# Optimization experiments

Measured on AMD Instinct MI355X. Metric: run time of the kernel, lower is better.

The kernel has to match this reference:

```python
import jax, jax.numpy as jnp
import numpy as np
from jax import lax

OUT_SIZE = 224  # original input spatial size (output_size of anomaly map)
NUM_NEIGHBORS = 9
SIGMA = 4.0
KSIZE = 2 * int(4.0 * SIGMA + 0.5) + 1  # 33, kornia-style kernel size


def avg_pool3(x):
    # AvgPool2d(3, 1, 1), count_include_pad=True -> sum over 3x3 window / 9
    s = lax.reduce_window(x, 0.0, lax.add, (1, 1, 3, 3), (1, 1, 1, 1),
                          [(0, 0), (0, 0), (1, 1), (1, 1)])
    return s / 9.0


def euclidean_dist(x, y):
    # x: [..., N, E], y: [..., M, E] -> [..., N, M]
    x_norm = jnp.sum(x * x, axis=-1, keepdims=True)
    y_norm = jnp.sum(y * y, axis=-1, keepdims=True)
    res = x_norm - 2.0 * jnp.matmul(x, jnp.swapaxes(y, -2, -1)) + jnp.swapaxes(y_norm, -2, -1)
    return jnp.sqrt(jnp.clip(res, 0.0))


def gaussian_blur(x):
    # x: [B,1,H,W]; separable Gaussian, reflect padding (kornia GaussianBlur2d default)
    r = KSIZE // 2
    t = jnp.arange(KSIZE, dtype=x.dtype) - r
    k = jnp.exp(-(t * t) / (2.0 * SIGMA * SIGMA))
    k = k / jnp.sum(k)
    xp = jnp.pad(x, ((0, 0), (0, 0), (r, r), (r, r)), mode='reflect')
    kh = k.reshape(1, 1, KSIZE, 1)
    kw = k.reshape(1, 1, 1, KSIZE)
    y = lax.conv_general_dilated(xp, kh, (1, 1), 'VALID',
                                 dimension_numbers=('NCHW', 'OIHW', 'NCHW'))
    return lax.conv_general_dilated(y, kw, (1, 1), 'VALID',
                                    dimension_numbers=('NCHW', 'OIHW', 'NCHW'))


def compute_anomaly_score(patch_scores, locations, embedding, memory_bank):
    # patch_scores/locations: [B, P]; embedding: [B*P, E]; memory_bank: [M, E]
    batch, num_patches = patch_scores.shape
    bidx = jnp.arange(batch)
    max_patches = jnp.argmax(patch_scores, axis=1)                       # [B]
    max_feats = embedding.reshape(batch, num_patches, -1)[bidx, max_patches]  # [B,E]
    score = patch_scores[bidx, max_patches]                              # [B]
    nn_index = locations[bidx, max_patches]                              # [B]
    nn_sample = memory_bank[nn_index]                                    # [B,E]
    n_nb = min(NUM_NEIGHBORS, memory_bank.shape[0])
    d_bank = euclidean_dist(nn_sample, memory_bank)                      # [B,M]
    _, support = lax.top_k(-d_bank, n_nb)                                # [B,k] smallest
    sup_feats = memory_bank[support]                                     # [B,k,E]
    d = euclidean_dist(max_feats[:, None, :], sup_feats)[:, 0, :]        # [B,k]
    weights = (1.0 - jax.nn.softmax(d, axis=1))[:, 0]                    # [B]
    return weights * score


def setup_inputs() -> dict:
    key = jax.random.key(0)
    k1, k2, k3 = jax.random.split(key, 3)
    feat2 = jax.random.normal(k1, (8, 512, 28, 28), dtype=jnp.float32)
    feat3 = jax.random.normal(k2, (8, 1024, 14, 14), dtype=jnp.float32)
    memory_bank = jax.random.normal(k3, (20000, 1536), dtype=jnp.float32)
    return {'feat2': feat2, 'feat3': feat3, 'memory_bank': memory_bank}


def reference(feat2, feat3, memory_bank):
    # feature pooling (AvgPool2d(3,1,1) on each backbone layer)
    f2 = avg_pool3(feat2)
    f3 = avg_pool3(feat3)
    batch, _, height, width = f2.shape
    # generate_embedding: bilinear upsample deeper layer, concat along channels
    f3u = jax.image.resize(f3, (batch, f3.shape[1], height, width), method='bilinear')
    emb = jnp.concatenate([f2, f3u], axis=1)                 # [B,1536,28,28]
    emb_dim = emb.shape[1]
    embedding = emb.transpose(0, 2, 3, 1).reshape(-1, emb_dim)  # [B*784, 1536]
    # nearest_neighbors with n_neighbors=1
    dist = euclidean_dist(embedding, memory_bank)            # [N, M]
    patch_scores = jnp.min(dist, axis=1)
    locations = jnp.argmin(dist, axis=1)
    patch_scores = patch_scores.reshape(batch, -1)
    locations = locations.reshape(batch, -1)
    pred_score = compute_anomaly_score(patch_scores, locations, embedding, memory_bank)
    # anomaly map: bilinear upsample patch scores to input size + gaussian blur
    score_map = patch_scores.reshape(batch, 1, width, height)
    amap = jax.image.resize(score_map, (batch, 1, OUT_SIZE, OUT_SIZE), method='bilinear')
    anomaly_map = gaussian_blur(amap)
    return anomaly_map, pred_score
```

## Files before the change

kernel.cpp:

```cpp
#include <hip/hip_runtime.h>
#include <math.h>

#define NB 8
#define C2 512
#define C3 1024
#define H2 28
#define W2 28
#define H3 14
#define W3 14
#define EDIM 1536
#define PPB (H2*W2)
#define NPATCH (NB*PPB)
#define MPAD 6400
#define MBANK 20000
#define NBPAD 20096
#define NBG (NBPAD/16)
#define OUTW 224
#define NNB 9
#define KS 33
#define KR 16
#define NMT 25
#define NNTB 157
#define CHUNKS 8
#define CH (MBANK/CHUNKS)
#define MPB 64
#define NSLAB 24
#define GRPB (NSLAB*1024)

#define SXQ 63.5f
#define SYQ (127.0f/6.0f)

typedef __attribute__((ext_vector_type(4))) int   i32x4;

#define LEXLT(va,ia,vb,ib) ((va) < (vb) || ((va)==(vb) && (ia)<(ib)))
#define CSWAP(va,ia,vb,ib) { if (LEXLT(va,ia,vb,ib)) { float _tv=(vb); int _ti=(ib); (vb)=(va); (ib)=(ia); (va)=_tv; (ia)=_ti; } }

#define BAR() asm volatile("s_barrier" ::: "memory")
#define WAITV6() asm volatile("s_waitcnt vmcnt(6)" ::: "memory")
#define WAITV0() asm volatile("s_waitcnt vmcnt(0)" ::: "memory")

__device__ __forceinline__ void gload16(const void* g, void* l) {
  __builtin_amdgcn_global_load_lds(
      (const __attribute__((address_space(1))) unsigned int*)g,
      (__attribute__((address_space(3))) unsigned int*)l, 16, 0, 0);
}
__device__ __forceinline__ signed char q8(float x, float s) {
  int v = (int)rintf(x * s);
  v = v > 127 ? 127 : (v < -127 ? -127 : v);
  return (signed char)v;
}
__device__ __forceinline__ size_t pk_addr(int row, int c) {
  return ((size_t)((row >> 4)*NSLAB + (c >> 6)) << 10)
       + (((c >> 4) & 3) << 8) + ((row & 15) << 4) + (c & 15);
}


__global__ __launch_bounds__(256) void pool2_kernel(const float* __restrict__ in,
    float* __restrict__ emb32, signed char* __restrict__ embp) {
  int bid = blockIdx.x;
  int cg = bid & 7; int h = (bid >> 3) % H2; int b = bid / (8*H2);
  int t = threadIdx.x;
  __shared__ float s3[3][64][29];
  for (int li = t; li < 3*64*28; li += 256) {
    int w = li % 28; int c = (li/28) & 63; int dh = li/(28*64);
    int hh = h + dh - 1;
    float v = 0.f;
    if (hh >= 0 && hh < H2) v = in[((size_t)(b*C2) + cg*64 + c)*784 + hh*28 + w];
    s3[dh][c][w] = v;
  }
  __syncthreads();
  for (int o = t; o < 64*28; o += 256) {
    int c = o & 63, w = o >> 6;
    float s = 0.f;
    #pragma unroll
    for (int dh = 0; dh < 3; ++dh) {
      s += s3[dh][c][w];
      if (w > 0)  s += s3[dh][c][w-1];
      if (w < 27) s += s3[dh][c][w+1];
    }
    s *= (1.f/9.f);
    int row = b*PPB + h*28 + w;
    int cc = cg*64 + c;
    emb32[(size_t)row*EDIM + cc] = s;
    embp[pk_addr(row, cc)] = q8(s, SXQ);
  }
}

__global__ void pool3_kernel(const float* __restrict__ in, float* __restrict__ f3p) {
  int id = blockIdx.x*blockDim.x + threadIdx.x;
  if (id >= NB*C3*H3*W3) return;
  int w = id % W3, h = (id / W3) % H3, c = (id / (H3*W3)) % C3, b = id / (C3*H3*W3);
  const float* src = in + (size_t)(b*C3 + c)*H3*W3;
  float s = 0.f;
  #pragma unroll
  for (int dh=-1; dh<=1; ++dh) {
    int hh = h+dh; if (hh<0||hh>=H3) continue;
    #pragma unroll
    for (int dw=-1; dw<=1; ++dw) {
      int ww = w+dw; if (ww<0||ww>=W3) continue;
      s += src[hh*W3+ww];
    }
  }
  f3p[(size_t)id] = s * (1.f/9.f);
}

__global__ __launch_bounds__(256) void up3_kernel(const float* __restrict__ f3p,
    float* __restrict__ emb32, signed char* __restrict__ embp) {
  int bid = blockIdx.x;
  int cg = bid & 15; int i = (bid >> 4) % H2; int b = bid / (16*H2);
  int t = threadIdx.x;
  float sy = i*0.5f - 0.25f; sy = fminf(fmaxf(sy,0.f),(float)(H3-1));
  int y0 = (int)sy; int y1 = min(y0+1,H3-1); float fy = sy - (float)y0;
  __shared__ float r2[2][64][15];
  for (int li = t; li < 2*64*14; li += 256) {
    int w = li % 14; int c = (li/14) & 63; int yy = li/(14*64);
    int ysrc = yy ? y1 : y0;
    r2[yy][c][w] = f3p[((size_t)(b*C3) + cg*64 + c)*196 + ysrc*14 + w];
  }
  __syncthreads();
  for (int o = t; o < 64*28; o += 256) {
    int c = o & 63, j = o >> 6;
    float sx = j*0.5f - 0.25f; sx = fminf(fmaxf(sx,0.f),(float)(W3-1));
    int x0 = (int)sx; int x1 = min(x0+1,W3-1); float fx = sx - (float)x0;
    float v = (1.f-fy)*((1.f-fx)*r2[0][c][x0] + fx*r2[0][c][x1])
            +      fy *((1.f-fx)*r2[1][c][x0] + fx*r2[1][c][x1]);
    int row = b*PPB + i*28 + j;
    int cc = C2 + cg*64 + c;
    emb32[(size_t)row*EDIM + cc] = v;
    embp[pk_addr(row, cc)] = q8(v, SXQ);
  }
}


__global__ __launch_bounds__(256) void bank_pack_kernel(const float* __restrict__ bank,
                                                        signed char* __restrict__ bankp,
                                                        float* __restrict__ yn) {
  __shared__ float rn[16];
  int grp = blockIdx.x;
  int t = threadIdx.x;
  if (t < 16) rn[t] = 0.f;
  __syncthreads();
  #pragma unroll
  for (int q = 0; q < 6; ++q) {
    int chunk = t + 256*q;
    int p = chunk >> 6, l = chunk & 63;
    int h = l & 15, gg = l >> 4;
    int row = grp*16 + h;
    int o16[4] = {0,0,0,0};
    if (row < MBANK) {
      const float* src = bank + (size_t)row*EDIM + p*64 + gg*16;
      signed char* oc = (signed char*)o16;
      float ls = 0.f;
      #pragma unroll
      for (int e = 0; e < 16; ++e) { float v = src[e]; ls = fmaf(v, v, ls); oc[e] = q8(v, SYQ); }
      atomicAdd(&rn[h], ls);
    }
    *reinterpret_cast<int4*>(bankp + (size_t)grp*GRPB + (size_t)chunk*16) =
        make_int4(o16[0], o16[1], o16[2], o16[3]);
  }
  __syncthreads();
  if (t < 16 && grp*16 + t < MBANK) yn[grp*16 + t] = rn[t];
}


__global__ __launch_bounds__(512, 4) void dist_min_i8(
    const signed char* __restrict__ Apk, const signed char* __restrict__ Bpk,
    const float* __restrict__ yn, float* __restrict__ outq, int* __restrict__ outi)
{
  __shared__ __align__(16) unsigned char LDSC[49152];
  const int t = threadIdx.x;
  const int lane = t & 63, wid = t >> 6;
  const int wr = wid >> 1, wc = wid & 1;

  const int nwg = NMT*NNTB;
  int orig = blockIdx.x;
  int xcd = orig & 7, loc = orig >> 3;
  int qq = nwg >> 3, rm = nwg & 7;
  int wg = (xcd < rm ? xcd*(qq+1) : rm*(qq+1) + (xcd-rm)*qq) + loc;
  const int mt = wg / NNTB, nt = wg % NNTB;
  const int m0 = mt*256, n0 = nt*128;

  const int gA = (m0 >> 4) + wid*2;
  const signed char* aSrc0 = Apk + (size_t)gA*GRPB + lane*16;
  const signed char* aSrc1 = Apk + (size_t)(gA+1)*GRPB + lane*16;
  const unsigned aDstOff = (unsigned)(wid*2048);

  const signed char* bp[4];
  #pragma unroll
  for (int j = 0; j < 4; ++j) {
    int n16 = (n0 >> 4) + wc*4 + j;
    bp[j] = Bpk + (size_t)n16*GRPB + lane*16;
  }
  const unsigned aRd = (unsigned)((wr*4)*1024 + lane*16);

  i32x4 acc[4][4];
  #pragma unroll
  for (int i = 0; i < 4; ++i)
    #pragma unroll
    for (int j = 0; j < 4; ++j) acc[i][j] = (i32x4){0,0,0,0};

  i32x4 bfv0[4], bfv1[4];

  gload16(aSrc0, (char*)LDSC + aDstOff);
  gload16(aSrc1, (char*)LDSC + aDstOff + 1024);
  gload16(aSrc0 + 1024, (char*)LDSC + 16384u + aDstOff);
  gload16(aSrc1 + 1024, (char*)LDSC + 16384u + aDstOff + 1024);
  #pragma unroll
  for (int j = 0; j < 4; ++j) bfv0[j] = *(const i32x4*)(bp[j]);
  WAITV6();
  BAR();

  #pragma unroll 2
  for (int p = 0; p < NSLAB; ++p) {
    const unsigned sb = (unsigned)(p % 3) * 16384u;
    const bool even = (p & 1) == 0;
    if (p < NSLAB-1) {
      if (even) {
        #pragma unroll
        for (int j = 0; j < 4; ++j) bfv1[j] = *(const i32x4*)(bp[j] + (size_t)(p+1)*1024);
      } else {
        #pragma unroll
        for (int j = 0; j < 4; ++j) bfv0[j] = *(const i32x4*)(bp[j] + (size_t)(p+1)*1024);
      }
    }
    if (p < NSLAB-2) {
      const unsigned sw = (unsigned)((p+2) % 3) * 16384u;
      gload16(aSrc0 + (size_t)(p+2)*1024, (char*)LDSC + sw + aDstOff);
      gload16(aSrc1 + (size_t)(p+2)*1024, (char*)LDSC + sw + aDstOff + 1024);
    }
    i32x4 af[4];
    #pragma unroll
    for (int i = 0; i < 4; ++i)
      af[i] = *(const i32x4*)(LDSC + sb + aRd + i*1024);
    __builtin_amdgcn_s_setprio(1);
    if (even) {
      #pragma unroll
      for (int i = 0; i < 4; ++i)
        #pragma unroll
        for (int j = 0; j < 4; ++j)
          acc[i][j] = __builtin_amdgcn_mfma_i32_16x16x64_i8(af[i], bfv0[j], acc[i][j], 0, 0, 0);
    } else {
      #pragma unroll
      for (int i = 0; i < 4; ++i)
        #pragma unroll
        for (int j = 0; j < 4; ++j)
          acc[i][j] = __builtin_amdgcn_mfma_i32_16x16x64_i8(af[i], bfv1[j], acc[i][j], 0, 0, 0);
    }
    __builtin_amdgcn_s_setprio(0);
    if (p < NSLAB-2) { WAITV6(); } else { WAITV0(); }
    BAR();
  }

  const float NEG2INV = -2.0f * (2.0f/127.0f) * (6.0f/127.0f);
  const int h = lane & 15, g = lane >> 4;
  float ynv[4];
  #pragma unroll
  for (int j = 0; j < 4; ++j) {
    int col = n0 + wc*64 + j*16 + h;
    ynv[j] = col < MBANK ? yn[col] : INFINITY;
  }
  float* smin = (float*)LDSC;
  int* sidx = (int*)(LDSC + 2048);
  #pragma unroll
  for (int i = 0; i < 4; ++i) {
    #pragma unroll
    for (int r = 0; r < 4; ++r) {
      float v = INFINITY; int ix = 0x7fffffff;
      #pragma unroll
      for (int j = 0; j < 4; ++j) {
        float q = fmaf(NEG2INV, (float)acc[i][j][r], ynv[j]);
        int col = n0 + wc*64 + j*16 + h;
        if (q < v || (q == v && col < ix)) { v = q; ix = col; }
      }
      #pragma unroll
      for (int m = 1; m < 16; m <<= 1) {
        float ov = __shfl_xor(v, m);
        int   oi = __shfl_xor(ix, m);
        if (ov < v || (ov == v && oi < ix)) { v = ov; ix = oi; }
      }
      if (h == 0) {
        int rl = wr*64 + i*16 + g*4 + r;
        smin[rl*2 + wc] = v;
        sidx[rl*2 + wc] = ix;
      }
    }
  }
  __syncthreads();
  if (t < 256) {
    float v0 = smin[t*2], v1 = smin[t*2+1];
    int   i0 = sidx[t*2], i1 = sidx[t*2+1];
    float v; int ix;
    if (LEXLT(v1, i1, v0, i0)) { v = v1; ix = i1; } else { v = v0; ix = i0; }
    int row = m0 + t;
    if (row < NPATCH) {
      outq[(size_t)nt*NPATCH + row] = v;
      outi[(size_t)nt*NPATCH + row] = ix;
    }
  }
}


__global__ __launch_bounds__(256) void minrescore_kernel(
    const float* __restrict__ outq, const int* __restrict__ outi,
    const float* __restrict__ emb32, const float* __restrict__ bank,
    const float* __restrict__ yn, int* __restrict__ loc, float* __restrict__ ps) {
  int w = (blockIdx.x*blockDim.x + threadIdx.x) >> 6;
  int lane = threadIdx.x & 63;
  if (w >= NPATCH) return;
  float bv = INFINITY; int bi = 0x7fffffff;
  for (int s = lane; s < NNTB; s += 64) {
    float v = outq[(size_t)s*NPATCH + w];
    int  ix = outi[(size_t)s*NPATCH + w];
    if (LEXLT(v, ix, bv, bi)) { bv = v; bi = ix; }
  }
  #pragma unroll
  for (int m = 32; m; m >>= 1) {
    float ov = __shfl_xor(bv, m);
    int   oi = __shfl_xor(bi, m);
    if (LEXLT(ov, oi, bv, bi)) { bv = ov; bi = oi; }
  }
  int j = bi;
  if (lane == 0) loc[w] = j;
  const float4* x = reinterpret_cast<const float4*>(emb32 + (size_t)w*EDIM);
  const float4* y = reinterpret_cast<const float4*>(bank + (size_t)j*EDIM);
  float accd = 0.f, accx = 0.f;
  #pragma unroll
  for (int k = 0; k < EDIM/4/64; ++k) {
    float4 a = x[lane + k*64], b = y[lane + k*64];
    accd = fmaf(a.x,b.x,accd); accd = fmaf(a.y,b.y,accd);
    accd = fmaf(a.z,b.z,accd); accd = fmaf(a.w,b.w,accd);
    accx = fmaf(a.x,a.x,accx); accx = fmaf(a.y,a.y,accx);
    accx = fmaf(a.z,a.z,accx); accx = fmaf(a.w,a.w,accx);
  }
  #pragma unroll
  for (int s = 32; s; s >>= 1) { accd += __shfl_xor(accd, s); accx += __shfl_xor(accx, s); }
  if (lane == 0) ps[w] = sqrtf(fmaxf(accx - 2.f*accd + yn[j], 0.f));
}


__global__ void argmax_kernel(const float* __restrict__ ps, const int* __restrict__ loc,
                              float* __restrict__ bscore, int* __restrict__ brow, int* __restrict__ bnn) {
  __shared__ float sv[256]; __shared__ int si[256];
  int b = blockIdx.x, t = threadIdx.x;
  float bv = -INFINITY; int bi = 0x7fffffff;
  for (int p = t; p < PPB; p += 256) {
    float v = ps[b*PPB + p];
    if (v > bv || (v == bv && p < bi)) { bv = v; bi = p; }
  }
  sv[t] = bv; si[t] = bi; __syncthreads();
  for (int s = 128; s; s >>= 1) {
    if (t < s) {
      if (sv[t+s] > sv[t] || (sv[t+s] == sv[t] && si[t+s] < si[t])) { sv[t] = sv[t+s]; si[t] = si[t+s]; }
    }
    __syncthreads();
  }
  if (t == 0) {
    bscore[b] = sv[0];
    brow[b]   = b*PPB + si[0];
    bnn[b]    = loc[b*PPB + si[0]];
  }
}

__global__ __launch_bounds__(256) void dbank_kernel(
    const float* __restrict__ bank, const float* __restrict__ yn,
    const int* __restrict__ bnn, float* __restrict__ dbank)
{
  __shared__ float xs[8][EDIM];
  int t = threadIdx.x;
  for (int idx = t*4; idx < 8*EDIM; idx += 256*4) {
    int b = idx / EDIM, k = idx % EDIM;
    float4 v = *reinterpret_cast<const float4*>(bank + (size_t)bnn[b]*EDIM + k);
    *reinterpret_cast<float4*>(&xs[b][k]) = v;
  }
  __syncthreads();
  int lane = t & 63, w = t >> 6;
  for (int u = 0; u < MPB/4; ++u) {
    int m = blockIdx.x*MPB + u*4 + w;
    if (m < MBANK) {
      const float4* yp = reinterpret_cast<const float4*>(bank + (size_t)m*EDIM);
      float acc[8] = {0.f,0.f,0.f,0.f,0.f,0.f,0.f,0.f};
      for (int k4 = lane; k4 < EDIM/4; k4 += 64) {
        float4 y = yp[k4];
        int k = k4*4;
        #pragma unroll
        for (int b = 0; b < 8; ++b) {
          acc[b] = fmaf(y.x, xs[b][k+0], acc[b]);
          acc[b] = fmaf(y.y, xs[b][k+1], acc[b]);
          acc[b] = fmaf(y.z, xs[b][k+2], acc[b]);
          acc[b] = fmaf(y.w, xs[b][k+3], acc[b]);
        }
      }
      #pragma unroll
      for (int b = 0; b < 8; ++b) {
        float a = acc[b];
        #pragma unroll
        for (int s = 32; s; s >>= 1) a += __shfl_xor(a, s);
        acc[b] = a;
      }
      if (lane == 0) {
        #pragma unroll
        for (int b = 0; b < 8; ++b) {
          int nn = bnn[b];
          float d2 = yn[nn] - 2.f*acc[b] + yn[m];
          dbank[(size_t)b*MBANK + m] = sqrtf(fmaxf(d2, 0.f));
        }
      }
    }
  }
}


__global__ __launch_bounds__(256) void top9_stage1(const float* __restrict__ dbank,
                                                   float* __restrict__ cv, int* __restrict__ ci) {
  int b = blockIdx.x / CHUNKS, ch = blockIdx.x % CHUNKS;
  const float* db = dbank + (size_t)b*MBANK + ch*CH;
  int t = threadIdx.x;

  float v0=INFINITY,v1=INFINITY,v2=INFINITY,v3=INFINITY,v4=INFINITY,
        v5=INFINITY,v6=INFINITY,v7=INFINITY,v8=INFINITY;
  int i0=0x7fffffff,i1=0x7fffffff,i2=0x7fffffff,i3=0x7fffffff,i4=0x7fffffff,
      i5=0x7fffffff,i6=0x7fffffff,i7=0x7fffffff,i8=0x7fffffff;

  for (int s = 0; s < (CH+255)/256; ++s) {
    int m = t + s*256;
    if (m < CH) {
      float nv = db[m]; int ni = ch*CH + m;
      if (LEXLT(nv,ni,v8,i8)) {
        v8 = nv; i8 = ni;
        CSWAP(v8,i8,v7,i7); CSWAP(v7,i7,v6,i6); CSWAP(v6,i6,v5,i5); CSWAP(v5,i5,v4,i4);
        CSWAP(v4,i4,v3,i3); CSWAP(v3,i3,v2,i2); CSWAP(v2,i2,v1,i1); CSWAP(v1,i1,v0,i0);
      }
    }
  }

  __shared__ float sv[256*9];
  __shared__ int   si[256*9];
  __shared__ float rv[256]; __shared__ int ri[256]; __shared__ int rp[256];
  sv[t*9+0]=v0; sv[t*9+1]=v1; sv[t*9+2]=v2; sv[t*9+3]=v3; sv[t*9+4]=v4;
  sv[t*9+5]=v5; sv[t*9+6]=v6; sv[t*9+7]=v7; sv[t*9+8]=v8;
  si[t*9+0]=i0; si[t*9+1]=i1; si[t*9+2]=i2; si[t*9+3]=i3; si[t*9+4]=i4;
  si[t*9+5]=i5; si[t*9+6]=i6; si[t*9+7]=i7; si[t*9+8]=i8;
  __syncthreads();

  for (int r = 0; r < NNB; ++r) {
    float bv = INFINITY; int bix = 0x7fffffff; int bp = -1;
    #pragma unroll
    for (int u = 0; u < 9; ++u) {
      float v = sv[t*9+u]; int ix = si[t*9+u];
      if (LEXLT(v,ix,bv,bix)) { bv = v; bix = ix; bp = t*9+u; }
    }
    rv[t] = bv; ri[t] = bix; rp[t] = bp; __syncthreads();
    for (int s = 128; s; s >>= 1) {
      if (t < s) {
        if (LEXLT(rv[t+s],ri[t+s],rv[t],ri[t])) { rv[t]=rv[t+s]; ri[t]=ri[t+s]; rp[t]=rp[t+s]; }
      }
      __syncthreads();
    }
    if (t == 0) {
      cv[blockIdx.x*NNB + r] = rv[0];
      ci[blockIdx.x*NNB + r] = ri[0];
      sv[rp[0]] = INFINITY; si[rp[0]] = 0x7fffffff;
    }
    __syncthreads();
  }
}


__global__ __launch_bounds__(128) void finalize_kernel(
    const float* __restrict__ cv, const int* __restrict__ ci,
    const float* __restrict__ emb32, const float* __restrict__ bank,
    const float* __restrict__ yn, const int* __restrict__ brow,
    const float* __restrict__ bscore, float* __restrict__ out) {
  __shared__ float sv[128]; __shared__ int si[128];
  __shared__ float wv[128]; __shared__ int wi[128]; __shared__ int wp[128];
  __shared__ int supp[NNB]; __shared__ float ds[NNB];
  int b = blockIdx.x, t = threadIdx.x;
  if (t < CHUNKS*NNB) { sv[t] = cv[b*CHUNKS*NNB + t]; si[t] = ci[b*CHUNKS*NNB + t]; }
  else { sv[t] = INFINITY; si[t] = 0x7fffffff; }
  __syncthreads();
  for (int r = 0; r < NNB; ++r) {
    wv[t] = sv[t]; wi[t] = si[t]; wp[t] = t; __syncthreads();
    for (int s = 64; s; s >>= 1) {
      if (t < s) {
        if (LEXLT(wv[t+s],wi[t+s],wv[t],wi[t])) { wv[t]=wv[t+s]; wi[t]=wi[t+s]; wp[t]=wp[t+s]; }
      }
      __syncthreads();
    }
    if (t == 0) {
      supp[r] = wi[0];
      sv[wp[0]] = INFINITY; si[wp[0]] = 0x7fffffff;
    }
    __syncthreads();
  }
  int lane = t & 63, w = t >> 6;
  int row = brow[b];
  const float* x = emb32 + (size_t)row*EDIM;
  for (int j = w; j < NNB; j += 2) {
    const float* y = bank + (size_t)supp[j]*EDIM;
    float accd = 0.f, accx = 0.f;
    for (int k = lane; k < EDIM; k += 64) {
      float a = x[k];
      accd = fmaf(a, y[k], accd);
      accx = fmaf(a, a, accx);
    }
    #pragma unroll
    for (int s = 32; s; s >>= 1) { accd += __shfl_xor(accd, s); accx += __shfl_xor(accx, s); }
    if (lane == 0) ds[j] = sqrtf(fmaxf(accx - 2.f*accd + yn[supp[j]], 0.f));
  }
  __syncthreads();
  if (t == 0) {
    float mx = -INFINITY;
    #pragma unroll
    for (int j = 0; j < NNB; ++j) mx = fmaxf(mx, ds[j]);
    float s = 0.f;
    #pragma unroll
    for (int j = 0; j < NNB; ++j) s += expf(ds[j] - mx);
    float wgt = 1.f - expf(ds[0] - mx) / s;
    out[b] = wgt * bscore[b];
  }
}


__device__ __forceinline__ int refl224(int x) {
  if (x < 0) return -x;
  if (x > OUTW-1) return 2*(OUTW-1) - x;
  return x;
}

__global__ __launch_bounds__(256) void upblurh_kernel(const float* __restrict__ ps,
                                                      float* __restrict__ tmp) {
  int b = blockIdx.x / OUTW, i = blockIdx.x % OUTW;
  int t = threadIdx.x;
  __shared__ float l[W2];
  __shared__ float graw[KS];
  if (t < KS) {
    float x = (float)t - (float)KR;
    graw[t] = expf(-(x*x) / (2.f*4.f*4.f));
  }
  float sy = ((float)i + 0.5f)*0.125f - 0.5f; sy = fminf(fmaxf(sy,0.f),(float)(H2-1));
  int y0 = (int)sy; int y1 = min(y0+1,H2-1); float fy = sy - (float)y0;
  if (t < W2) {
    const float* p = ps + b*PPB;
    l[t] = (1.f-fy)*p[y0*W2+t] + fy*p[y1*W2+t];
  }
  __syncthreads();
  if (t >= OUTW) return;
  float gsum = 0.f;
  #pragma unroll
  for (int u = 0; u < KS; ++u) gsum += graw[u];
  float winv = 1.f / gsum;
  float s = 0.f;
  #pragma unroll
  for (int v = 0; v < KS; ++v) {
    int jj = refl224(t - KR + v);
    float sx = ((float)jj + 0.5f)*0.125f - 0.5f; sx = fminf(fmaxf(sx,0.f),(float)(W2-1));
    int x0 = (int)sx; int x1 = min(x0+1,W2-1); float fx = sx - (float)x0;
    s = fmaf(graw[v]*winv, (1.f-fx)*l[x0] + fx*l[x1], s);
  }
  tmp[((size_t)b*OUTW + i)*OUTW + t] = s;
}

__global__ __launch_bounds__(256) void blurv_kernel(const float* __restrict__ in,
                                                    float* __restrict__ out) {
  __shared__ float graw[KS];
  int t = threadIdx.x;
  if (t < KS) {
    float x = (float)t - (float)KR;
    graw[t] = expf(-(x*x) / (2.f*4.f*4.f));
  }
  __syncthreads();
  int id = blockIdx.x*blockDim.x + t;
  if (id >= NB*OUTW*OUTW) return;
  float gsum = 0.f;
  #pragma unroll
  for (int u = 0; u < KS; ++u) gsum += graw[u];
  float winv = 1.f / gsum;
  int j = id % OUTW, i = (id/OUTW) % OUTW, b = id/(OUTW*OUTW);
  float s = 0.f;
  #pragma unroll
  for (int u = 0; u < KS; ++u) {
    int ii = refl224(i - KR + u);
    s = fmaf(graw[u]*winv, in[((size_t)b*OUTW + ii)*OUTW + j], s);
  }
  out[id] = s;
}


extern "C" void kernel_launch(void* const* d_in, const int* in_sizes, int n_in,
                              void* d_out, int out_size, void* d_ws, size_t ws_size,
                              hipStream_t stream) {
  const float* feat2 = (const float*)d_in[0];
  const float* feat3 = (const float*)d_in[1];
  const float* bank  = (const float*)d_in[2];
  float* out = (float*)d_out;

  char* base = (char*)d_ws;
  size_t off = 0;
  auto alloc = [&](size_t nbytes) -> char* {
    char* p = base + off;
    off += ((nbytes + 255) & ~(size_t)255);
    return p;
  };
  float*       emb32 = (float*)      alloc((size_t)NPATCH*EDIM*4);
  signed char* embp  = (signed char*)alloc((size_t)(MPAD/16)*GRPB);
  signed char* bankp = (signed char*)alloc((size_t)NBG*GRPB);
  float* f3p    = (float*)alloc((size_t)NB*C3*H3*W3*4);
  float* yn     = (float*)alloc(MBANK*4);
  float* outq   = (float*)alloc((size_t)NNTB*NPATCH*4);
  int*   outi   = (int*)  alloc((size_t)NNTB*NPATCH*4);
  float* ps     = (float*)alloc(NPATCH*4);
  int*   loc    = (int*)  alloc(NPATCH*4);
  float* bscore = (float*)alloc(NB*4);
  int*   brow   = (int*)  alloc(NB*4);
  int*   bnn    = (int*)  alloc(NB*4);
  float* dbank  = (float*)alloc((size_t)NB*MBANK*4);
  float* cv     = (float*)alloc(NB*CHUNKS*NNB*4);
  int*   ci     = (int*)  alloc(NB*CHUNKS*NNB*4);
  float* tmp    = (float*)alloc((size_t)NB*OUTW*OUTW*4);

  pool2_kernel<<<NB*H2*8, 256, 0, stream>>>(feat2, emb32, embp);
  {
    int n = NB*C3*H3*W3;
    pool3_kernel<<<(n+255)/256, 256, 0, stream>>>(feat3, f3p);
  }
  up3_kernel<<<NB*H2*16, 256, 0, stream>>>(f3p, emb32, embp);
  bank_pack_kernel<<<NBG, 256, 0, stream>>>(bank, bankp, yn);

  dist_min_i8<<<NMT*NNTB, 512, 0, stream>>>(embp, bankp, yn, outq, outi);
  minrescore_kernel<<<(NPATCH*64)/256, 256, 0, stream>>>(outq, outi, emb32, bank, yn, loc, ps);

  argmax_kernel<<<NB, 256, 0, stream>>>(ps, loc, bscore, brow, bnn);
  dbank_kernel<<<(MBANK+MPB-1)/MPB, 256, 0, stream>>>(bank, yn, bnn, dbank);
  top9_stage1<<<NB*CHUNKS, 256, 0, stream>>>(dbank, cv, ci);
  finalize_kernel<<<NB, 128, 0, stream>>>(cv, ci, emb32, bank, yn, brow, bscore,
                                          out + NB*OUTW*OUTW);

  {
    upblurh_kernel<<<NB*OUTW, 256, 0, stream>>>(ps, tmp);
    int n = NB*OUTW*OUTW;
    blurv_kernel<<<(n+255)/256, 256, 0, stream>>>(tmp, out);
  }
}
```

Before: 485.5 us.

## Fuse argmax into rescore via atomic keys and fuse dbank with per-block top-9

Replaces the separate per-batch argmax kernel with a packed 64-bit atomicMax issued from the rescore kernel. The bank-distance computation is fused with a per-block top-9 selection, so the 8x20000 distance matrix is never written to global memory. The two-stage top-9 merge is collapsed into the finalize kernel. This removes two launches and one global round trip, but adds atomics, a memset, and a larger candidate list (313 blocks x 9) for finalize to merge serially.

```diff
diff --git a/kernel.cpp b/kernel.cpp
--- a/kernel.cpp
+++ b/kernel.cpp
@@ -21,8 +21,7 @@
 #define KR 16
 #define NMT 25
 #define NNTB 157
-#define CHUNKS 8
-#define CH (MBANK/CHUNKS)
+#define NBLK 313
 #define MPB 64
 #define NSLAB 24
 #define GRPB (NSLAB*1024)
@@ -174,9 +173,9 @@
 
   const int nwg = NMT*NNTB;
   int orig = blockIdx.x;
-  int xcd = orig & 7, loc = orig >> 3;
+  int xcd = orig & 7, loc_ = orig >> 3;
   int qq = nwg >> 3, rm = nwg & 7;
-  int wg = (xcd < rm ? xcd*(qq+1) : rm*(qq+1) + (xcd-rm)*qq) + loc;
+  int wg = (xcd < rm ? xcd*(qq+1) : rm*(qq+1) + (xcd-rm)*qq) + loc_;
   const int mt = wg / NNTB, nt = wg % NNTB;
   const int m0 = mt*256, n0 = nt*128;
 
@@ -303,7 +302,8 @@
 __global__ __launch_bounds__(256) void minrescore_kernel(
     const float* __restrict__ outq, const int* __restrict__ outi,
     const float* __restrict__ emb32, const float* __restrict__ bank,
-    const float* __restrict__ yn, int* __restrict__ loc, float* __restrict__ ps) {
+    const float* __restrict__ yn, int* __restrict__ loc, float* __restrict__ ps,
+    unsigned long long* __restrict__ keys) {
   int w = (blockIdx.x*blockDim.x + threadIdx.x) >> 6;
   int lane = threadIdx.x & 63;
   if (w >= NPATCH) return;
@@ -320,7 +320,6 @@
     if (LEXLT(ov, oi, bv, bi)) { bv = ov; bi = oi; }
   }
   int j = bi;
-  if (lane == 0) loc[w] = j;
   const float4* x = reinterpret_cast<const float4*>(emb32 + (size_t)w*EDIM);
   const float4* y = reinterpret_cast<const float4*>(bank + (size_t)j*EDIM);
   float accd = 0.f, accx = 0.f;
@@ -334,48 +333,43 @@
   }
   #pragma unroll
   for (int s = 32; s; s >>= 1) { accd += __shfl_xor(accd, s); accx += __shfl_xor(accx, s); }
-  if (lane == 0) ps[w] = sqrtf(fmaxf(accx - 2.f*accd + yn[j], 0.f));
-}
-
-
-__global__ void argmax_kernel(const float* __restrict__ ps, const int* __restrict__ loc,
-                              float* __restrict__ bscore, int* __restrict__ brow, int* __restrict__ bnn) {
-  __shared__ float sv[256]; __shared__ int si[256];
-  int b = blockIdx.x, t = threadIdx.x;
-  float bv = -INFINITY; int bi = 0x7fffffff;
-  for (int p = t; p < PPB; p += 256) {
-    float v = ps[b*PPB + p];
-    if (v > bv || (v == bv && p < bi)) { bv = v; bi = p; }
-  }
-  sv[t] = bv; si[t] = bi; __syncthreads();
-  for (int s = 128; s; s >>= 1) {
-    if (t < s) {
-      if (sv[t+s] > sv[t] || (sv[t+s] == sv[t] && si[t+s] < si[t])) { sv[t] = sv[t+s]; si[t] = si[t+s]; }
-    }
-    __syncthreads();
-  }
-  if (t == 0) {
-    bscore[b] = sv[0];
-    brow[b]   = b*PPB + si[0];
-    bnn[b]    = loc[b*PPB + si[0]];
-  }
-}
-
-__global__ __launch_bounds__(256) void dbank_kernel(
+  if (lane == 0) {
+    float d = sqrtf(fmaxf(accx - 2.f*accd + yn[j], 0.f));
+    loc[w] = j;
+    ps[w] = d;
+    int b = w / PPB, p = w % PPB;
+    unsigned long long key = ((unsigned long long)__float_as_uint(d) << 32)
+                           | (unsigned)(0x7fffffff - p);
+    atomicMax(&keys[b], key);
+  }
+}
+
+
+__global__ __launch_bounds__(256) void dbank_top9_kernel(
     const float* __restrict__ bank, const float* __restrict__ yn,
-    const int* __restrict__ bnn, float* __restrict__ dbank)
+    const unsigned long long* __restrict__ keys, const int* __restrict__ loc,
+    float* __restrict__ cv, int* __restrict__ ci)
 {
   __shared__ float xs[8][EDIM];
+  __shared__ float dsv[8][64];
+  __shared__ int bnnl[8];
   int t = threadIdx.x;
+  if (t < 8) {
+    unsigned long long k = keys[t];
+    int p = 0x7fffffff - (int)(unsigned)(k & 0xffffffffu);
+    bnnl[t] = loc[t*PPB + p];
+  }
+  __syncthreads();
   for (int idx = t*4; idx < 8*EDIM; idx += 256*4) {
     int b = idx / EDIM, k = idx % EDIM;
-    float4 v = *reinterpret_cast<const float4*>(bank + (size_t)bnn[b]*EDIM + k);
+    float4 v = *reinterpret_cast<const float4*>(bank + (size_t)bnnl[b]*EDIM + k);
     *reinterpret_cast<float4*>(&xs[b][k]) = v;
   }
   __syncthreads();
   int lane = t & 63, w = t >> 6;
-  for (int u = 0; u < MPB/4; ++u) {
-    int m = blockIdx.x*MPB + u*4 + w;
+  for (int u = 0; u < 16; ++u) {
+    int ri = u*4 + w;
+    int m = blockIdx.x*64 + ri;
     if (m < MBANK) {
       const float4* yp = reinterpret_cast<const float4*>(bank + (size_t)m*EDIM);
       float acc[8] = {0.f,0.f,0.f,0.f,0.f,0.f,0.f,0.f};
@@ -400,48 +394,70 @@
       if (lane == 0) {
         #pragma unroll
         for (int b = 0; b < 8; ++b) {
-          int nn = bnn[b];
-          float d2 = yn[nn] - 2.f*acc[b] + yn[m];
-          dbank[(size_t)b*MBANK + m] = sqrtf(fmaxf(d2, 0.f));
+          float d2 = yn[bnnl[b]] - 2.f*acc[b] + yn[m];
+          dsv[b][ri] = sqrtf(fmaxf(d2, 0.f));
         }
       }
-    }
-  }
-}
-
-
-__global__ __launch_bounds__(256) void top9_stage1(const float* __restrict__ dbank,
-                                                   float* __restrict__ cv, int* __restrict__ ci) {
-  int b = blockIdx.x / CHUNKS, ch = blockIdx.x % CHUNKS;
-  const float* db = dbank + (size_t)b*MBANK + ch*CH;
-  int t = threadIdx.x;
+    } else if (lane == 0) {
+      #pragma unroll
+      for (int b = 0; b < 8; ++b) dsv[b][ri] = INFINITY;
+    }
+  }
+  __syncthreads();
+  #pragma unroll
+  for (int bb = 0; bb < 2; ++bb) {
+    int b = w*2 + bb;
+    float val = dsv[b][lane];
+    int idx = blockIdx.x*64 + lane;
+    if (idx >= MBANK) { val = INFINITY; idx = 0x7fffffff; }
+    for (int r = 0; r < NNB; ++r) {
+      float v = val; int ix = idx;
+      #pragma unroll
+      for (int m = 1; m < 64; m <<= 1) {
+        float ov = __shfl_xor(v, m);
+        int   oi = __shfl_xor(ix, m);
+        if (LEXLT(ov, oi, v, ix)) { v = ov; ix = oi; }
+      }
+      if (lane == 0) {
+        cv[((size_t)b*NBLK + blockIdx.x)*NNB + r] = v;
+        ci[((size_t)b*NBLK + blockIdx.x)*NNB + r] = ix;
+      }
+      if (idx == ix) { val = INFINITY; idx = 0x7fffffff; }
+    }
+  }
+}
+
+
+__global__ __launch_bounds__(256) void finalize_kernel(
+    const float* __restrict__ cv, const int* __restrict__ ci,
+    const float* __restrict__ emb32, const float* __restrict__ bank,
+    const float* __restrict__ yn, const int* __restrict__ loc,
+    const unsigned long long* __restrict__ keys, const float* __restrict__ ps,
+    float* __restrict__ out) {
+  __shared__ float sv[256*9];
+  __shared__ int   si[256*9];
+  __shared__ float rv[256]; __shared__ int ri[256]; __shared__ int rp[256];
+  __shared__ int supp[NNB]; __shared__ float ds[NNB];
+  int b = blockIdx.x, t = threadIdx.x;
 
   float v0=INFINITY,v1=INFINITY,v2=INFINITY,v3=INFINITY,v4=INFINITY,
         v5=INFINITY,v6=INFINITY,v7=INFINITY,v8=INFINITY;
   int i0=0x7fffffff,i1=0x7fffffff,i2=0x7fffffff,i3=0x7fffffff,i4=0x7fffffff,
       i5=0x7fffffff,i6=0x7fffffff,i7=0x7fffffff,i8=0x7fffffff;
-
-  for (int s = 0; s < (CH+255)/256; ++s) {
-    int m = t + s*256;
-    if (m < CH) {
-      float nv = db[m]; int ni = ch*CH + m;
-      if (LEXLT(nv,ni,v8,i8)) {
-        v8 = nv; i8 = ni;
-        CSWAP(v8,i8,v7,i7); CSWAP(v7,i7,v6,i6); CSWAP(v6,i6,v5,i5); CSWAP(v5,i5,v4,i4);
-        CSWAP(v4,i4,v3,i3); CSWAP(v3,i3,v2,i2); CSWAP(v2,i2,v1,i1); CSWAP(v1,i1,v0,i0);
-      }
-    }
-  }
-
-  __shared__ float sv[256*9];
-  __shared__ int   si[256*9];
-  __shared__ float rv[256]; __shared__ int ri[256]; __shared__ int rp[256];
+  for (int e = t; e < NBLK*NNB; e += 256) {
+    float nv = cv[(size_t)b*NBLK*NNB + e];
+    int   ni = ci[(size_t)b*NBLK*NNB + e];
+    if (LEXLT(nv,ni,v8,i8)) {
+      v8 = nv; i8 = ni;
+      CSWAP(v8,i8,v7,i7); CSWAP(v7,i7,v6,i6); CSWAP(v6,i6,v5,i5); CSWAP(v5,i5,v4,i4);
+      CSWAP(v4,i4,v3,i3); CSWAP(v3,i3,v2,i2); CSWAP(v2,i2,v1,i1); CSWAP(v1,i1,v0,i0);
+    }
+  }
   sv[t*9+0]=v0; sv[t*9+1]=v1; sv[t*9+2]=v2; sv[t*9+3]=v3; sv[t*9+4]=v4;
   sv[t*9+5]=v5; sv[t*9+6]=v6; sv[t*9+7]=v7; sv[t*9+8]=v8;
   si[t*9+0]=i0; si[t*9+1]=i1; si[t*9+2]=i2; si[t*9+3]=i3; si[t*9+4]=i4;
   si[t*9+5]=i5; si[t*9+6]=i6; si[t*9+7]=i7; si[t*9+8]=i8;
   __syncthreads();
-
   for (int r = 0; r < NNB; ++r) {
     float bv = INFINITY; int bix = 0x7fffffff; int bp = -1;
     #pragma unroll
@@ -457,45 +473,16 @@
       __syncthreads();
     }
     if (t == 0) {
-      cv[blockIdx.x*NNB + r] = rv[0];
-      ci[blockIdx.x*NNB + r] = ri[0];
+      supp[r] = ri[0];
       sv[rp[0]] = INFINITY; si[rp[0]] = 0x7fffffff;
     }
     __syncthreads();
   }
-}
-
-
-__global__ __launch_bounds__(128) void finalize_kernel(
-    const float* __restrict__ cv, const int* __restrict__ ci,
-    const float* __restrict__ emb32, const float* __restrict__ bank,
-    const float* __restrict__ yn, const int* __restrict__ brow,
-    const float* __restrict__ bscore, float* __restrict__ out) {
-  __shared__ float sv[128]; __shared__ int si[128];
-  __shared__ float wv[128]; __shared__ int wi[128]; __shared__ int wp[128];
-  __shared__ int supp[NNB]; __shared__ float ds[NNB];
-  int b = blockIdx.x, t = threadIdx.x;
-  if (t < CHUNKS*NNB) { sv[t] = cv[b*CHUNKS*NNB + t]; si[t] = ci[b*CHUNKS*NNB + t]; }
-  else { sv[t] = INFINITY; si[t] = 0x7fffffff; }
-  __syncthreads();
-  for (int r = 0; r < NNB; ++r) {
-    wv[t] = sv[t]; wi[t] = si[t]; wp[t] = t; __syncthreads();
-    for (int s = 64; s; s >>= 1) {
-      if (t < s) {
-        if (LEXLT(wv[t+s],wi[t+s],wv[t],wi[t])) { wv[t]=wv[t+s]; wi[t]=wi[t+s]; wp[t]=wp[t+s]; }
-      }
-      __syncthreads();
-    }
-    if (t == 0) {
-      supp[r] = wi[0];
-      sv[wp[0]] = INFINITY; si[wp[0]] = 0x7fffffff;
-    }
-    __syncthreads();
-  }
   int lane = t & 63, w = t >> 6;
-  int row = brow[b];
+  int p = 0x7fffffff - (int)(unsigned)(keys[b] & 0xffffffffu);
+  int row = b*PPB + p;
   const float* x = emb32 + (size_t)row*EDIM;
-  for (int j = w; j < NNB; j += 2) {
+  for (int j = w; j < NNB; j += 4) {
     const float* y = bank + (size_t)supp[j]*EDIM;
     float accd = 0.f, accx = 0.f;
     for (int k = lane; k < EDIM; k += 64) {
@@ -516,7 +503,7 @@
     #pragma unroll
     for (int j = 0; j < NNB; ++j) s += expf(ds[j] - mx);
     float wgt = 1.f - expf(ds[0] - mx) / s;
-    out[b] = wgt * bscore[b];
+    out[b] = wgt * ps[row];
   }
 }
 
@@ -610,13 +597,12 @@
   int*   outi   = (int*)  alloc((size_t)NNTB*NPATCH*4);
   float* ps     = (float*)alloc(NPATCH*4);
   int*   loc    = (int*)  alloc(NPATCH*4);
-  float* bscore = (float*)alloc(NB*4);
-  int*   brow   = (int*)  alloc(NB*4);
-  int*   bnn    = (int*)  alloc(NB*4);
-  float* dbank  = (float*)alloc((size_t)NB*MBANK*4);
-  float* cv     = (float*)alloc(NB*CHUNKS*NNB*4);
-  int*   ci     = (int*)  alloc(NB*CHUNKS*NNB*4);
+  unsigned long long* keys = (unsigned long long*)alloc(NB*8);
+  float* cv     = (float*)alloc((size_t)NB*NBLK*NNB*4);
+  int*   ci     = (int*)  alloc((size_t)NB*NBLK*NNB*4);
   float* tmp    = (float*)alloc((size_t)NB*OUTW*OUTW*4);
+
+  hipMemsetAsync(keys, 0, NB*8, stream);
 
   pool2_kernel<<<NB*H2*8, 256, 0, stream>>>(feat2, emb32, embp);
   {
@@ -627,12 +613,11 @@
   bank_pack_kernel<<<NBG, 256, 0, stream>>>(bank, bankp, yn);
 
   dist_min_i8<<<NMT*NNTB, 512, 0, stream>>>(embp, bankp, yn, outq, outi);
-  minrescore_kernel<<<(NPATCH*64)/256, 256, 0, stream>>>(outq, outi, emb32, bank, yn, loc, ps);
-
-  argmax_kernel<<<NB, 256, 0, stream>>>(ps, loc, bscore, brow, bnn);
-  dbank_kernel<<<(MBANK+MPB-1)/MPB, 256, 0, stream>>>(bank, yn, bnn, dbank);
-  top9_stage1<<<NB*CHUNKS, 256, 0, stream>>>(dbank, cv, ci);
-  finalize_kernel<<<NB, 128, 0, stream>>>(cv, ci, emb32, bank, yn, brow, bscore,
+  minrescore_kernel<<<(NPATCH*64)/256, 256, 0, stream>>>(outq, outi, emb32, bank, yn,
+                                                         loc, ps, keys);
+
+  dbank_top9_kernel<<<NBLK, 256, 0, stream>>>(bank, yn, keys, loc, cv, ci);
+  finalize_kernel<<<NB, 256, 0, stream>>>(cv, ci, emb32, bank, yn, loc, keys, ps,
                                           out + NB*OUTW*OUTW);
 
   {
```

Result: slower. 537.2 us (+10.7%).
